# Performance work log

Measured on AMD Instinct MI355X. Metric: run time of the kernel, lower is better.

Reference implementation:

```python
import jax, jax.numpy as jnp
import numpy as np

D_K = 64  # per-head dim, hardcoded in the original module


def setup_inputs() -> dict:
    key = jax.random.key(0)
    kq, kk, kv, km = jax.random.split(key, 4)
    B, H, S, D = 4, 16, 2048, 64
    Q = jax.random.normal(kq, (B, H, S, D), dtype=jnp.float32)
    K = jax.random.normal(kk, (B, H, S, D), dtype=jnp.float32)
    V = jax.random.normal(kv, (B, H, S, D), dtype=jnp.float32)
    attn_mask = jax.random.randint(km, (B, H, S, S), 0, 2).astype(jnp.bool_)
    return {"Q": Q, "K": K, "V": V, "attn_mask": attn_mask}


def reference(Q, K, V, attn_mask):
    # scores = Q @ K^T / sqrt(d_k)  -> [B, H, S, S]
    scale = 1.0 / np.sqrt(D_K).astype(np.float32)
    scores = jnp.einsum("bhqd,bhkd->bhqk", Q, K) * scale
    scores = jnp.where(attn_mask, jnp.float32(-1e9), scores)
    attn = jax.nn.softmax(scores, axis=-1)
    context = jnp.einsum("bhqk,bhkd->bhqd", attn, V)
    return (context, attn)
```

## Files before the change

### kernel.cpp

```cpp
#include <hip/hip_runtime.h>
#include <hip/hip_bf16.h>
#include <stdint.h>

#define S_LEN 2048
#define D_HEAD 64
#define NBH 64
#define QBLK 64
#define KBLK 64
#define NITER (S_LEN / KBLK)

#define QSCALE 0.1803368801111244f

typedef __attribute__((ext_vector_type(8))) short short8;
typedef __attribute__((ext_vector_type(4))) float f32x4;

#define KB_OFF   0
#define VT_OFF   24576
#define PRED_OFF 40960
#define P_OFF    57344
#define LP_OFF   57344
#define SMEM_BYTES 65536

#define FK_OFF  0
#define FVT_OFF 16384
#define FP_OFF  24576
#define FMB_OFF 28672
#define FLP_OFF 36864
#define FSMEM_BYTES 37120

__device__ __forceinline__ int swz1(int row, int b) {
  return row * 128 + (b ^ ((row & 7) << 4));
}
__device__ __forceinline__ int swz2(int row, int b) {
  return row * 128 + (b ^ (((row >> 1) & 7) << 4));
}

__device__ __forceinline__ short f2b(float x) {
  unsigned u = __float_as_uint(x);
  unsigned r = 0x7FFFu + ((u >> 16) & 1u);
  return (short)((u + r) >> 16);
}
__device__ __forceinline__ float b2f(short s) {
  return __uint_as_float(((unsigned)(unsigned short)s) << 16);
}

__device__ __forceinline__ void gload_lds16(const void* g, void* l) {
  __builtin_amdgcn_global_load_lds(
      (const __attribute__((address_space(1))) unsigned int*)g,
      (__attribute__((address_space(3))) unsigned int*)l, 16, 0, 0);
}

#define WAITBAR(N) do { \
  asm volatile("s_waitcnt vmcnt(" #N ") lgkmcnt(0)" ::: "memory"); \
  __builtin_amdgcn_s_barrier(); } while (0)
#define LGKMBAR() do { \
  asm volatile("s_waitcnt lgkmcnt(0)" ::: "memory"); \
  __builtin_amdgcn_s_barrier(); } while (0)

__global__ void detect_mask_kernel(const unsigned* m, int* flag) {
  unsigned v = m[blockIdx.x * 256 + threadIdx.x];
  if (v != 0u && v != 1u && v != 0x3F800000u) atomicOr(flag, 1);
}

__global__ void __launch_bounds__(256) convK_kernel(
    const float* __restrict__ in, short* __restrict__ out) {
  size_t i = ((size_t)blockIdx.x * 256 + threadIdx.x) * 8;
  float4 a = ((const float4*)(in + i))[0];
  float4 b = ((const float4*)(in + i))[1];
  short8 v;
  v[0] = f2b(a.x); v[1] = f2b(a.y); v[2] = f2b(a.z); v[3] = f2b(a.w);
  v[4] = f2b(b.x); v[5] = f2b(b.y); v[6] = f2b(b.z); v[7] = f2b(b.w);
  *(short8*)(out + i) = v;
}

__global__ void __launch_bounds__(256) convVT_kernel(
    const float* __restrict__ V, short* __restrict__ out) {
  __shared__ __align__(16) short t[64 * 72];
  int tid = threadIdx.x;
  int kb = blockIdx.x * 64, bh = blockIdx.y;
  const float* src = V + ((size_t)bh * S_LEN + kb) * D_HEAD;
#pragma unroll
  for (int j = 0; j < 4; ++j) {
    int key = j * 16 + (tid >> 4), d0 = (tid & 15) * 4;
    float4 f = *(const float4*)(src + (size_t)key * D_HEAD + d0);
    t[(d0 + 0) * 72 + key] = f2b(f.x);
    t[(d0 + 1) * 72 + key] = f2b(f.y);
    t[(d0 + 2) * 72 + key] = f2b(f.z);
    t[(d0 + 3) * 72 + key] = f2b(f.w);
  }
  __syncthreads();
  int row = tid >> 2, seg = tid & 3;
  short8 v0 = *(const short8*)(t + row * 72 + seg * 16);
  short8 v1 = *(const short8*)(t + row * 72 + seg * 16 + 8);
  short* dst = out + (size_t)bh * D_HEAD * S_LEN + (size_t)row * S_LEN + kb + seg * 16;
  *(short8*)dst = v0;
  *(short8*)(dst + 8) = v1;
}

template <bool BYTEMASK>
__device__ __forceinline__ void attn_fast(
    char* smem, const float* __restrict__ Qg, const void* __restrict__ maskg,
    const short* __restrict__ Kbf, const short* __restrict__ Vtb,
    float* __restrict__ ctxg, float* __restrict__ attng,
    int qb, int bh) {

  const int tid = threadIdx.x;
  const int w = tid >> 6, l = tid & 63;
  const int lg = l >> 4, li = l & 15;
  const int rh = w >> 1, ch = w & 1;
  const int qbase = qb * QBLK;
  const int row = tid >> 3, seg = tid & 7;

  const float* Qp = Qg + ((size_t)bh * S_LEN + qbase) * D_HEAD;
  const short* Kbp = Kbf + (size_t)bh * S_LEN * D_HEAD;
  const short* Vtp = Vtb + (size_t)bh * D_HEAD * S_LEN;
  float* attnp = attng + ((size_t)bh * S_LEN + qbase) * S_LEN;
  float* ctxp  = ctxg  + ((size_t)bh * S_LEN + qbase) * D_HEAD;
  const size_t mbase = ((size_t)bh * S_LEN + qbase + row) * S_LEN + seg * 8;

  auto stageK = [&](int it) {
    const int buf = it % 3;
    const short* src = Kbp + ((size_t)(it * KBLK + row)) * D_HEAD + ((seg ^ (row & 7)) * 8);
    int off = __builtin_amdgcn_readfirstlane(buf * 8192 + w * 1024);
    gload_lds16(src, smem + KB_OFF + off);
  };
  auto stageVt = [&](int it) {
    const int buf = it & 1;
    const short* src = Vtp + (size_t)row * S_LEN + it * KBLK + ((seg ^ (row & 7)) * 8);
    int off = __builtin_amdgcn_readfirstlane(buf * 8192 + w * 1024);
    gload_lds16(src, smem + VT_OFF + off);
  };

  auto qkt = [&](f32x4* accs, const short8* qf, int it) {
    char* kb = smem + KB_OFF + (it % 3) * 8192;
#pragma unroll
    for (int ct = 0; ct < 2; ++ct) {
      int key = ch * 32 + ct * 16 + li;
      short8 b0 = *(const short8*)(kb + swz1(key, lg * 16));
      short8 b1 = *(const short8*)(kb + swz1(key, 64 + lg * 16));
      accs[ct] = __builtin_amdgcn_mfma_f32_16x16x32_bf16(qf[0], b0, accs[ct], 0, 0, 0);
      accs[ct] = __builtin_amdgcn_mfma_f32_16x16x32_bf16(qf[1], b1, accs[ct], 0, 0, 0);
    }
  };

  struct MaskRegs { int4 a, b; uint2 c; };
  auto loadMask = [&](int it, MaskRegs& m) {
    if constexpr (BYTEMASK) {
      m.c = *(const uint2*)((const unsigned char*)maskg + mbase + it * KBLK);
    } else {
      const int* p = (const int*)maskg + mbase + it * KBLK;
      m.a = *(const int4*)p;
      m.b = *(const int4*)(p + 4);
    }
  };
  auto predWrite = [&](int it, const MaskRegs& m) {
    unsigned pb = 0;
    if constexpr (BYTEMASK) {
      unsigned lo = m.c.x, hi = m.c.y;
#pragma unroll
      for (int j = 0; j < 4; ++j) {
        pb |= (((lo >> (8 * j)) & 255u) != 0u ? 1u : 0u) << j;
        pb |= (((hi >> (8 * j)) & 255u) != 0u ? 1u : 0u) << (j + 4);
      }
    } else {
      pb |= (m.a.x != 0) ? 1u : 0u;
      pb |= (m.a.y != 0) ? 2u : 0u;
      pb |= (m.a.z != 0) ? 4u : 0u;
      pb |= (m.a.w != 0) ? 8u : 0u;
      pb |= (m.b.x != 0) ? 16u : 0u;
      pb |= (m.b.y != 0) ? 32u : 0u;
      pb |= (m.b.z != 0) ? 64u : 0u;
      pb |= (m.b.w != 0) ? 128u : 0u;
    }
    *(unsigned char*)(smem + PRED_OFF + it * 512 + row * 8 + seg) = (unsigned char)pb;
  };

  MaskRegs t0, t1, mA, mB;
  loadMask(0, t0); loadMask(1, t1); loadMask(2, mA); loadMask(3, mB);
  stageK(0); stageK(1);
  {
    const float* src = Qp + row * D_HEAD + seg * 8;
    float4 a = ((const float4*)src)[0];
    float4 b = ((const float4*)src)[1];
    short8 v;
    v[0] = f2b(a.x * QSCALE); v[1] = f2b(a.y * QSCALE);
    v[2] = f2b(a.z * QSCALE); v[3] = f2b(a.w * QSCALE);
    v[4] = f2b(b.x * QSCALE); v[5] = f2b(b.y * QSCALE);
    v[6] = f2b(b.z * QSCALE); v[7] = f2b(b.w * QSCALE);
    *(short8*)(smem + P_OFF + swz1(row, seg * 16)) = v;
  }
  __syncthreads();
  short8 qfrag[2];
  {
    int qr = rh * 16 + li;
    qfrag[0] = *(const short8*)(smem + P_OFF + swz1(qr, lg * 16));
    qfrag[1] = *(const short8*)(smem + P_OFF + swz1(qr, 64 + lg * 16));
  }
  predWrite(0, t0);
  predWrite(1, t1);

  float l_acc[4] = {0.f, 0.f, 0.f, 0.f};
  auto p1iter = [&](int i, MaskRegs& m) {
    f32x4 accs[2] = {{0.f,0.f,0.f,0.f},{0.f,0.f,0.f,0.f}};
    qkt(accs, qfrag, i);
    if (i <= 27) {
      if constexpr (BYTEMASK) WAITBAR(1); else WAITBAR(2);
    } else {
      WAITBAR(0);
    }
    if (i + 2 < NITER) stageK(i + 2);
    if (i + 2 < NITER) predWrite(i + 2, m);
    if (i + 4 < NITER) loadMask(i + 4, m);
#pragma unroll
    for (int reg = 0; reg < 4; ++reg) {
      int rw = rh * 16 + lg * 4 + reg;
      unsigned long long p64 =
          *(const unsigned long long*)(smem + PRED_OFF + i * 512 + rw * 8);
      unsigned pw = (unsigned)(p64 >> (ch << 5));
      float e0 = ((pw >> li) & 1u)        ? 0.f : exp2f(accs[0][reg]);
      float e1 = ((pw >> (16 + li)) & 1u) ? 0.f : exp2f(accs[1][reg]);
      l_acc[reg] += e0 + e1;
    }
  };
  for (int i = 0; i < NITER; i += 2) {
    p1iter(i, mA);
    p1iter(i + 1, mB);
  }

#pragma unroll
  for (int reg = 0; reg < 4; ++reg) {
    float s = l_acc[reg];
    s += __shfl_xor(s, 1);
    s += __shfl_xor(s, 2);
    s += __shfl_xor(s, 4);
    s += __shfl_xor(s, 8);
    l_acc[reg] = s;
  }
  if (li == 0) {
#pragma unroll
    for (int reg = 0; reg < 4; ++reg)
      *(float*)(smem + LP_OFF + ch * 256 + (rh * 16 + lg * 4 + reg) * 4) = l_acc[reg];
  }
  stageK(0); stageK(1); stageVt(0);
  WAITBAR(0);
  float linv[4];
#pragma unroll
  for (int reg = 0; reg < 4; ++reg) {
    int rw = rh * 16 + lg * 4 + reg;
    linv[reg] = 1.0f / (*(const float*)(smem + LP_OFF + rw * 4) +
                        *(const float*)(smem + LP_OFF + 256 + rw * 4));
  }
  float* arow = attnp + (size_t)row * S_LEN + seg * 8;

  f32x4 acco[2] = {{0.f,0.f,0.f,0.f},{0.f,0.f,0.f,0.f}};
  for (int i = 0; i < NITER; ++i) {
    f32x4 accs[2] = {{0.f,0.f,0.f,0.f},{0.f,0.f,0.f,0.f}};
    qkt(accs, qfrag, i);
    LGKMBAR();
    if (i + 2 < NITER) stageK(i + 2);
    if (i + 1 < NITER) stageVt(i + 1);
#pragma unroll
    for (int reg = 0; reg < 4; ++reg) {
      int rw = rh * 16 + lg * 4 + reg;
      unsigned long long p64 =
          *(const unsigned long long*)(smem + PRED_OFF + i * 512 + rw * 8);
      unsigned pw = (unsigned)(p64 >> (ch << 5));
      float e0 = ((pw >> li) & 1u)        ? 0.f : exp2f(accs[0][reg]) * linv[reg];
      float e1 = ((pw >> (16 + li)) & 1u) ? 0.f : exp2f(accs[1][reg]) * linv[reg];
      *(short*)(smem + P_OFF + swz2(rw, (ch * 32 + li) * 2)) = f2b(e0);
      *(short*)(smem + P_OFF + swz2(rw, (ch * 32 + 16 + li) * 2)) = f2b(e1);
    }
    if (i == 0) WAITBAR(2);
    else if (i <= 29) WAITBAR(4);
    else if (i == 30) WAITBAR(3);
    else WAITBAR(2);
    {
      short8 pv = *(const short8*)(smem + P_OFF + swz2(row, seg * 16));
      float4 f0, f1;
      f0.x = b2f(pv[0]); f0.y = b2f(pv[1]); f0.z = b2f(pv[2]); f0.w = b2f(pv[3]);
      f1.x = b2f(pv[4]); f1.y = b2f(pv[5]); f1.z = b2f(pv[6]); f1.w = b2f(pv[7]);
      ((float4*)(arow + i * KBLK))[0] = f0;
      *(float4*)(arow + i * KBLK + 4) = f1;
    }
    {
      char* vb = smem + VT_OFF + (i & 1) * 8192;
#pragma unroll
      for (int ks = 0; ks < 2; ++ks) {
        int prow = rh * 16 + li;
        short8 af = *(const short8*)(smem + P_OFF + swz2(prow, ks * 64 + lg * 16));
#pragma unroll
        for (int ct2 = 0; ct2 < 2; ++ct2) {
          int d = ch * 32 + ct2 * 16 + li;
          short8 bf = *(const short8*)(vb + swz1(d, ks * 64 + lg * 16));
          acco[ct2] = __builtin_amdgcn_mfma_f32_16x16x32_bf16(af, bf, acco[ct2], 0, 0, 0);
        }
      }
    }
  }

#pragma unroll
  for (int ct2 = 0; ct2 < 2; ++ct2)
#pragma unroll
    for (int reg = 0; reg < 4; ++reg) {
      int rw = rh * 16 + lg * 4 + reg;
      int d = ch * 32 + ct2 * 16 + li;
      ctxp[(size_t)rw * D_HEAD + d] = acco[ct2][reg];
    }
}

__global__ void __launch_bounds__(512, 4)
attn_fast_kernel(const float* Q, const void* M, const short* Kbf, const short* Vtb,
                 float* ctx, float* attn, const int* flag) {
  __shared__ __align__(16) char smem[SMEM_BYTES];
  int bid = blockIdx.x;
  int s = ((bid & 7) << 8) | (bid >> 3);
  int bh = s >> 5, qb = s & 31;
  if (*flag)
    attn_fast<true>(smem, Q, M, Kbf, Vtb, ctx, attn, qb, bh);
  else
    attn_fast<false>(smem, Q, M, Kbf, Vtb, ctx, attn, qb, bh);
}

template <bool BYTEMASK>
__device__ __forceinline__ void attn_body(
    char* smem, const float* Qg, const float* Kg, const float* Vg,
    const void* maskg, float* ctxg, float* attng) {

  const int tid = threadIdx.x;
  const int w = tid >> 6, l = tid & 63;
  const int lg = l >> 4, li = l & 15;
  const int rh = w >> 1, ch = w & 1;
  const int qb = blockIdx.x, bh = blockIdx.y;
  const int qbase = qb * 32;

  const float* Qp = Qg + ((size_t)bh * S_LEN + qbase) * D_HEAD;
  const float* Kp = Kg + (size_t)bh * S_LEN * D_HEAD;
  const float* Vp = Vg + (size_t)bh * S_LEN * D_HEAD;
  float* attnp = attng + ((size_t)bh * S_LEN + qbase) * S_LEN;
  float* ctxp  = ctxg  + ((size_t)bh * S_LEN + qbase) * D_HEAD;
  const size_t mrow0 = ((size_t)bh * S_LEN + qbase) * S_LEN;

  auto stageK = [&](int it, int buf) {
    char* kb = smem + FK_OFF + buf * 8192;
    int key = tid >> 2, seg = tid & 3;
    const float* src = Kp + ((size_t)(it * KBLK + key)) * D_HEAD + seg * 16;
    float4 f0 = ((const float4*)src)[0];
    float4 f1 = ((const float4*)src)[1];
    float4 f2 = ((const float4*)src)[2];
    float4 f3 = ((const float4*)src)[3];
    short8 v0, v1;
    v0[0] = f2b(f0.x); v0[1] = f2b(f0.y); v0[2] = f2b(f0.z); v0[3] = f2b(f0.w);
    v0[4] = f2b(f1.x); v0[5] = f2b(f1.y); v0[6] = f2b(f1.z); v0[7] = f2b(f1.w);
    v1[0] = f2b(f2.x); v1[1] = f2b(f2.y); v1[2] = f2b(f2.z); v1[3] = f2b(f2.w);
    v1[4] = f2b(f3.x); v1[5] = f2b(f3.y); v1[6] = f2b(f3.z); v1[7] = f2b(f3.w);
    *(short8*)(kb + swz1(key, seg * 32)) = v0;
    *(short8*)(kb + swz1(key, seg * 32 + 16)) = v1;
  };

  auto stageVt = [&](int it) {
    char* vb = smem + FVT_OFF;
    int key = l, db = w;
    const float* src = Vp + ((size_t)(it * KBLK + key)) * D_HEAD + db * 16;
#pragma unroll
    for (int j = 0; j < 4; ++j) {
      float4 f = ((const float4*)src)[j];
      int dd = db * 16 + j * 4;
      *(short*)(vb + swz1(dd + 0, key * 2)) = f2b(f.x);
      *(short*)(vb + swz1(dd + 1, key * 2)) = f2b(f.y);
      *(short*)(vb + swz1(dd + 2, key * 2)) = f2b(f.z);
      *(short*)(vb + swz1(dd + 3, key * 2)) = f2b(f.w);
    }
  };

  auto loadMask = [&](int it, unsigned* m) {
#pragma unroll
    for (int reg = 0; reg < 4; ++reg) {
      int rw = rh * 16 + lg * 4 + reg;
#pragma unroll
      for (int ct = 0; ct < 2; ++ct) {
        size_t idx = mrow0 + (size_t)rw * S_LEN + it * KBLK + ch * 32 + ct * 16 + li;
        if constexpr (BYTEMASK)
          m[ct * 4 + reg] = (unsigned)((const unsigned char*)maskg)[idx];
        else
          m[ct * 4 + reg] = ((const unsigned*)maskg)[idx];
      }
    }
  };

  auto qkt = [&](f32x4* accs, const short8* qf, int buf) {
    char* kb = smem + FK_OFF + buf * 8192;
#pragma unroll
    for (int ct = 0; ct < 2; ++ct) {
      int key = ch * 32 + ct * 16 + li;
      short8 b0 = *(const short8*)(kb + swz1(key, lg * 16));
      short8 b1 = *(const short8*)(kb + swz1(key, 64 + lg * 16));
      accs[ct] = __builtin_amdgcn_mfma_f32_16x16x32_bf16(qf[0], b0, accs[ct], 0, 0, 0);
      accs[ct] = __builtin_amdgcn_mfma_f32_16x16x32_bf16(qf[1], b1, accs[ct], 0, 0, 0);
    }
  };

  stageK(0, 0);
  unsigned mc[8];
  loadMask(0, mc);
  {
    int rw = tid >> 3, seg = tid & 7;
    const float* src = Qp + rw * D_HEAD + seg * 8;
    float4 a = ((const float4*)src)[0];
    float4 b = ((const float4*)src)[1];
    short8 v;
    v[0] = f2b(a.x); v[1] = f2b(a.y); v[2] = f2b(a.z); v[3] = f2b(a.w);
    v[4] = f2b(b.x); v[5] = f2b(b.y); v[6] = f2b(b.z); v[7] = f2b(b.w);
    *(short8*)(smem + FP_OFF + swz1(rw, seg * 16)) = v;
  }
  __syncthreads();
  short8 qfrag[2];
  {
    int rw = rh * 16 + li;
    qfrag[0] = *(const short8*)(smem + FP_OFF + swz1(rw, lg * 16));
    qfrag[1] = *(const short8*)(smem + FP_OFF + swz1(rw, 64 + lg * 16));
  }
  __syncthreads();

  float l_acc[4] = {0.f, 0.f, 0.f, 0.f};
  for (int it = 0; it < NITER; ++it) {
    const int cb = it & 1, nb = cb ^ 1;
    if (it + 1 < NITER) stageK(it + 1, nb);
    unsigned mn[8];
    if (it + 1 < NITER) loadMask(it + 1, mn);
    f32x4 accs[2] = {{0.f,0.f,0.f,0.f},{0.f,0.f,0.f,0.f}};
    qkt(accs, qfrag, cb);
    unsigned mbyte = 0;
#pragma unroll
    for (int reg = 0; reg < 4; ++reg) {
      float contrib = 0.f;
#pragma unroll
      for (int ct = 0; ct < 2; ++ct) {
        bool pred = mc[ct * 4 + reg] != 0u;
        mbyte |= (unsigned)pred << (ct * 4 + reg);
        float pp = pred ? 0.f : __expf(accs[ct][reg] * 0.125f);
        contrib += pp;
      }
      contrib += __shfl_xor(contrib, 1);
      contrib += __shfl_xor(contrib, 2);
      contrib += __shfl_xor(contrib, 4);
      contrib += __shfl_xor(contrib, 8);
      l_acc[reg] += contrib;
    }
    *(unsigned char*)(smem + FMB_OFF + it * 256 + tid) = (unsigned char)mbyte;
    __syncthreads();
    if (it + 1 < NITER) {
#pragma unroll
      for (int i = 0; i < 8; ++i) mc[i] = mn[i];
    }
  }

  if (li == 0) {
#pragma unroll
    for (int reg = 0; reg < 4; ++reg)
      *(float*)(smem + FLP_OFF + ch * 128 + (rh * 16 + lg * 4 + reg) * 4) = l_acc[reg];
  }
  stageK(0, 0);
  stageVt(0);
  __syncthreads();
  float linv[4];
#pragma unroll
  for (int reg = 0; reg < 4; ++reg) {
    int rw = rh * 16 + lg * 4 + reg;
    linv[reg] = 1.0f / (*(const float*)(smem + FLP_OFF + rw * 4) +
                        *(const float*)(smem + FLP_OFF + 128 + rw * 4));
  }

  f32x4 acco[2] = {{0.f,0.f,0.f,0.f},{0.f,0.f,0.f,0.f}};
  for (int it = 0; it < NITER; ++it) {
    const int cb = it & 1, nb = cb ^ 1;
    if (it > 0) stageVt(it);
    if (it + 1 < NITER) stageK(it + 1, nb);
    f32x4 accs[2] = {{0.f,0.f,0.f,0.f},{0.f,0.f,0.f,0.f}};
    qkt(accs, qfrag, cb);
    unsigned mbyte = *(const unsigned char*)(smem + FMB_OFF + it * 256 + tid);
#pragma unroll
    for (int reg = 0; reg < 4; ++reg) {
      int rw = rh * 16 + lg * 4 + reg;
#pragma unroll
      for (int ct = 0; ct < 2; ++ct) {
        int col = ch * 32 + ct * 16 + li;
        bool pred = (mbyte >> (ct * 4 + reg)) & 1u;
        float pp = pred ? 0.f : __expf(accs[ct][reg] * 0.125f) * linv[reg];
        attnp[(size_t)rw * S_LEN + it * KBLK + col] = pp;
        *(short*)(smem + FP_OFF + swz2(rw, col * 2)) = f2b(pp);
      }
    }
    __syncthreads();
#pragma unroll
    for (int ks = 0; ks < 2; ++ks) {
      int prow = rh * 16 + li;
      short8 af = *(const short8*)(smem + FP_OFF + swz2(prow, ks * 64 + lg * 16));
#pragma unroll
      for (int ct2 = 0; ct2 < 2; ++ct2) {
        int d = ch * 32 + ct2 * 16 + li;
        short8 bf = *(const short8*)(smem + FVT_OFF + swz1(d, ks * 64 + lg * 16));
        acco[ct2] = __builtin_amdgcn_mfma_f32_16x16x32_bf16(af, bf, acco[ct2], 0, 0, 0);
      }
    }
    __syncthreads();
  }

#pragma unroll
  for (int ct2 = 0; ct2 < 2; ++ct2) {
#pragma unroll
    for (int reg = 0; reg < 4; ++reg) {
      int rw = rh * 16 + lg * 4 + reg;
      int d = ch * 32 + ct2 * 16 + li;
      ctxp[(size_t)rw * D_HEAD + d] = acco[ct2][reg];
    }
  }
}

__global__ void __launch_bounds__(256, 4)
attn_kernel(const float* Q, const float* K, const float* V, const void* M,
            float* ctx, float* attn, const int* flag) {
  extern __shared__ char smem[];
  if (*flag)
    attn_body<true>(smem, Q, K, V, M, ctx, attn);
  else
    attn_body<false>(smem, Q, K, V, M, ctx, attn);
}

extern "C" void kernel_launch(void* const* d_in, const int* in_sizes, int n_in,
                              void* d_out, int out_size, void* d_ws, size_t ws_size,
                              hipStream_t stream) {
  const float* Q = (const float*)d_in[0];
  const float* K = (const float*)d_in[1];
  const float* V = (const float*)d_in[2];
  const void*  M = d_in[3];
  float* ctx  = (float*)d_out;
  float* attn = ctx + (size_t)NBH * S_LEN * D_HEAD;
  int* flag = (int*)d_ws;
  short* Kbf = (short*)((char*)d_ws + 256);
  short* Vtb = Kbf + (size_t)NBH * S_LEN * D_HEAD;
  const size_t PRE_BYTES = 256 + (size_t)2 * NBH * S_LEN * D_HEAD * sizeof(short);

  hipMemsetAsync(flag, 0, sizeof(int), stream);
  detect_mask_kernel<<<dim3(16), dim3(256), 0, stream>>>((const unsigned*)M, flag);

  if (ws_size >= PRE_BYTES) {
    convK_kernel<<<dim3(4096), dim3(256), 0, stream>>>(K, Kbf);
    convVT_kernel<<<dim3(32, 64), dim3(256), 0, stream>>>(V, Vtb);
    attn_fast_kernel<<<dim3(2048), dim3(512), 0, stream>>>(
        Q, M, Kbf, Vtb, ctx, attn, flag);
  } else {
    dim3 grid(S_LEN / 32, NBH);
    attn_kernel<<<grid, dim3(256), FSMEM_BYTES, stream>>>(
        Q, K, V, M, ctx, attn, flag);
  }
}
```

Baseline: 567.7 us.

## Shrink LDS footprint by single-buffering V and double-buffering K for occupancy

Cuts the fast kernel's shared-memory allocation from 64KB to 48KB. The second pass now double-buffers K instead of triple-buffering it, and loads the V tile into a single buffer during the same iteration instead of prefetching it one step ahead. The first pass still uses three K slots, and the third slot overlaps the V region, which is idle at that point. Launch bounds rise to six waves per SIMD. The aim is to fit more workgroups per CU to hide memory latency on this bandwidth-heavy kernel, at the cost of a shallower prefetch pipeline and a tighter register budget that could cause spills.

```diff
diff --git a/kernel.cpp b/kernel.cpp
--- a/kernel.cpp
+++ b/kernel.cpp
@@ -15,11 +15,11 @@
 typedef __attribute__((ext_vector_type(4))) float f32x4;
 
 #define KB_OFF   0
-#define VT_OFF   24576
-#define PRED_OFF 40960
-#define P_OFF    57344
-#define LP_OFF   57344
-#define SMEM_BYTES 65536
+#define VT_OFF   16384
+#define PRED_OFF 24576
+#define P_OFF    40960
+#define LP_OFF   40960
+#define SMEM_BYTES 49152
 
 #define FK_OFF  0
 #define FVT_OFF 16384
@@ -118,21 +118,19 @@
   float* ctxp  = ctxg  + ((size_t)bh * S_LEN + qbase) * D_HEAD;
   const size_t mbase = ((size_t)bh * S_LEN + qbase + row) * S_LEN + seg * 8;
 
-  auto stageK = [&](int it) {
-    const int buf = it % 3;
+  auto stageK = [&](int it, int buf) {
     const short* src = Kbp + ((size_t)(it * KBLK + row)) * D_HEAD + ((seg ^ (row & 7)) * 8);
     int off = __builtin_amdgcn_readfirstlane(buf * 8192 + w * 1024);
     gload_lds16(src, smem + KB_OFF + off);
   };
   auto stageVt = [&](int it) {
-    const int buf = it & 1;
     const short* src = Vtp + (size_t)row * S_LEN + it * KBLK + ((seg ^ (row & 7)) * 8);
-    int off = __builtin_amdgcn_readfirstlane(buf * 8192 + w * 1024);
+    int off = __builtin_amdgcn_readfirstlane(w * 1024);
     gload_lds16(src, smem + VT_OFF + off);
   };
 
-  auto qkt = [&](f32x4* accs, const short8* qf, int it) {
-    char* kb = smem + KB_OFF + (it % 3) * 8192;
+  auto qkt = [&](f32x4* accs, const short8* qf, int buf) {
+    char* kb = smem + KB_OFF + buf * 8192;
 #pragma unroll
     for (int ct = 0; ct < 2; ++ct) {
       int key = ch * 32 + ct * 16 + li;
@@ -177,7 +175,7 @@
 
   MaskRegs t0, t1, mA, mB;
   loadMask(0, t0); loadMask(1, t1); loadMask(2, mA); loadMask(3, mB);
-  stageK(0); stageK(1);
+  stageK(0, 0); stageK(1, 1);
   {
     const float* src = Qp + row * D_HEAD + seg * 8;
     float4 a = ((const float4*)src)[0];
@@ -202,13 +200,13 @@
   float l_acc[4] = {0.f, 0.f, 0.f, 0.f};
   auto p1iter = [&](int i, MaskRegs& m) {
     f32x4 accs[2] = {{0.f,0.f,0.f,0.f},{0.f,0.f,0.f,0.f}};
-    qkt(accs, qfrag, i);
+    qkt(accs, qfrag, i % 3);
     if (i <= 27) {
       if constexpr (BYTEMASK) WAITBAR(1); else WAITBAR(2);
     } else {
       WAITBAR(0);
     }
-    if (i + 2 < NITER) stageK(i + 2);
+    if (i + 2 < NITER) stageK(i + 2, (i + 2) % 3);
     if (i + 2 < NITER) predWrite(i + 2, m);
     if (i + 4 < NITER) loadMask(i + 4, m);
 #pragma unroll
@@ -241,7 +239,7 @@
     for (int reg = 0; reg < 4; ++reg)
       *(float*)(smem + LP_OFF + ch * 256 + (rh * 16 + lg * 4 + reg) * 4) = l_acc[reg];
   }
-  stageK(0); stageK(1); stageVt(0);
+  stageK(0, 0); stageK(1, 1);
   WAITBAR(0);
   float linv[4];
 #pragma unroll
@@ -255,10 +253,10 @@
   f32x4 acco[2] = {{0.f,0.f,0.f,0.f},{0.f,0.f,0.f,0.f}};
   for (int i = 0; i < NITER; ++i) {
     f32x4 accs[2] = {{0.f,0.f,0.f,0.f},{0.f,0.f,0.f,0.f}};
-    qkt(accs, qfrag, i);
+    qkt(accs, qfrag, i & 1);
     LGKMBAR();
-    if (i + 2 < NITER) stageK(i + 2);
-    if (i + 1 < NITER) stageVt(i + 1);
+    stageVt(i);
+    if (i + 2 < NITER) stageK(i + 2, (i + 2) & 1);
 #pragma unroll
     for (int reg = 0; reg < 4; ++reg) {
       int rw = rh * 16 + lg * 4 + reg;
@@ -270,10 +268,7 @@
       *(short*)(smem + P_OFF + swz2(rw, (ch * 32 + li) * 2)) = f2b(e0);
       *(short*)(smem + P_OFF + swz2(rw, (ch * 32 + 16 + li) * 2)) = f2b(e1);
     }
-    if (i == 0) WAITBAR(2);
-    else if (i <= 29) WAITBAR(4);
-    else if (i == 30) WAITBAR(3);
-    else WAITBAR(2);
+    if (i + 2 < NITER) WAITBAR(1); else WAITBAR(0);
     {
       short8 pv = *(const short8*)(smem + P_OFF + swz2(row, seg * 16));
       float4 f0, f1;
@@ -283,7 +278,7 @@
       *(float4*)(arow + i * KBLK + 4) = f1;
     }
     {
-      char* vb = smem + VT_OFF + (i & 1) * 8192;
+      char* vb = smem + VT_OFF;
 #pragma unroll
       for (int ks = 0; ks < 2; ++ks) {
         int prow = rh * 16 + li;
@@ -308,7 +303,7 @@
     }
 }
 
-__global__ void __launch_bounds__(512, 4)
+__global__ void __launch_bounds__(512, 6)
 attn_fast_kernel(const float* Q, const void* M, const short* Kbf, const short* Vtb,
                  float* ctx, float* attn, const int* flag) {
   __shared__ __align__(16) char smem[SMEM_BYTES];
```

Result: slower. 673.2 us (+18.6%).
